# Optimization experiments

Measured on AMD Instinct MI355X. Metric: run time of the kernel, lower is better.

Reference implementation:

```python
import jax, jax.numpy as jnp
import numpy as np

B, C, D, T = 64, 1024, 32, 32
F4 = C // 4
GLOBAL_MARGIN = 0.2
MAX_VIOLATION = True
EPS = 1e-8


def setup_inputs() -> dict:
    key = jax.random.key(0)
    k = jax.random.split(key, 8)
    videos = jax.random.normal(k[0], (B, C, D, T), jnp.float32)
    sentences = jax.random.normal(k[1], (B, C), jnp.float32)
    lam = jnp.full((1,), 0.3, jnp.float32)
    mask = jnp.ones((B, D, T), jnp.int32)
    iou_maps = jax.random.uniform(k[2], (D * T, D * T), dtype=jnp.float32)
    lim = float(np.sqrt(6.0 / (C + F4)))  # xavier_uniform for Linear(C, C//4)
    W_v = jax.random.uniform(k[3], (4, C, F4), jnp.float32, -lim, lim)
    b_v = jnp.zeros((4, F4), jnp.float32)
    W_s = jax.random.uniform(k[4], (4, C, F4), jnp.float32, -lim, lim)
    b_s = jnp.zeros((4, F4), jnp.float32)
    return dict(videos=videos, sentences=sentences, lam=lam, mask=mask,
                iou_maps=iou_maps, valid_num=50,
                W_v=W_v, b_v=b_v, W_s=W_s, b_s=b_s)


def _forward(videos, sentences, W_v, b_v, W_s, b_s, lam, mask, iou_maps, valid_num):
    b, c, d, t = videos.shape
    # per-sample channel-mean centering
    videos = videos - jnp.mean(videos, axis=1, keepdims=True)
    sentences = sentences - jnp.mean(sentences, axis=1, keepdims=True)
    # 4-way linear projections, concatenated back along channel dim
    v = jnp.transpose(videos, (0, 2, 3, 1))                      # [b,d,t,c]
    v_cat = (jnp.einsum('bdtc,kcf->bkfdt', v, W_v)
             + b_v[None, :, :, None, None]).reshape(b, c, d, t)  # [b,c,d,t]
    s_cat = (jnp.einsum('bc,kcf->bkf', sentences, W_s) + b_s[None]).reshape(b, c)
    # cosine similarity over channel dim, vectorized over the batch loop
    vn = v_cat / jnp.maximum(jnp.linalg.norm(v_cat, axis=1, keepdims=True), EPS)
    sn = s_cat / jnp.maximum(jnp.linalg.norm(s_cat, axis=1, keepdims=True), EPS)
    sim = jnp.einsum('bcdt,sc->sbdt', vn, sn)                    # [s,b,d,t]
    sim = jnp.where(mask[None] == 0, -jnp.inf, sim)
    positive_map = sim[jnp.arange(b), jnp.arange(b)]             # [b,d,t]
    # top-k proposals + soft-NMS suppression (get_video_score_nms)
    flat = sim.reshape(b, b, d * t)
    vals, idx = jax.lax.top_k(flat, valid_num)                   # [s,b,v]
    iou_sub = iou_maps[idx[..., :, None], idx[..., None, :]]     # [s,b,v,v]
    tril = jnp.tril(jnp.ones((valid_num, valid_num), vals.dtype), -1)
    penalty = jnp.einsum('sblk,lk->sbk', iou_sub * iou_sub, tril)
    w = jnp.exp(-penalty / lam[0])                               # gaussian soft-NMS weight
    scores = jnp.mean(vals * w, axis=-1)                         # [s,b]
    # margin-based contrastive loss on the b x b score matrix
    diag = jnp.diagonal(scores)
    cost_s = jnp.clip(GLOBAL_MARGIN + scores - diag[:, None], 0.0)
    cost_im = jnp.clip(GLOBAL_MARGIN + scores - diag[None, :], 0.0)
    eye = jnp.eye(b, dtype=bool)
    cost_s = jnp.where(eye, 0.0, cost_s)
    cost_im = jnp.where(eye, 0.0, cost_im)
    if MAX_VIOLATION:
        cost_s = cost_s.max(axis=1)
        cost_im = cost_im.max(axis=0)
    loss = cost_s.sum() / b + cost_im.sum() / b
    return loss, positive_map


def reference(videos, sentences, lam, mask, iou_maps, valid_num, W_v, b_v, W_s, b_s):
    return _forward(videos, sentences, W_v, b_v, W_s, b_s, lam, mask, iou_maps, valid_num)
```

## Files before the change

kernel.cpp:

```cpp
#include <hip/hip_runtime.h>
#include <cstdint>
#include <cstddef>

#define CDIM  1024
#define DTDIM 1024
#define MDIM  65536
#define BDIM  64
#define VNUM  50

typedef __attribute__((ext_vector_type(8))) short bf16x8;
typedef __attribute__((ext_vector_type(4))) float f32x4;

__device__ __forceinline__ float bf2f(unsigned int u16) {
  return __uint_as_float(u16 << 16);
}
__device__ __forceinline__ unsigned short f2bf(float x) {
  unsigned int u = __float_as_uint(x);
  u += 0x7fffu + ((u >> 16) & 1u);
  return (unsigned short)(u >> 16);
}

__device__ __forceinline__ void gload16(const void* g, void* l) {
  __builtin_amdgcn_global_load_lds((const __attribute__((address_space(1))) void*)g,
                                   (__attribute__((address_space(3))) void*)l,
                                   16, 0, 0);
}

__global__ void k_transpose_videos(const float* __restrict__ vid,
                                   unsigned short* __restrict__ At,
                                   float* __restrict__ vsums) {
  __shared__ float t[64][65];
  const int tid = threadIdx.x;
  const int dt0 = blockIdx.x * 64, c0 = blockIdx.y * 64, b = blockIdx.z;
  const int lc = tid >> 4;
  const int l4 = (tid & 15) * 4;
  const float* src = vid + ((size_t)b * CDIM + c0) * DTDIM + dt0;
#pragma unroll
  for (int p = 0; p < 4; p++) {
    const int c = p * 16 + lc;
    const float4 f = *reinterpret_cast<const float4*>(&src[(size_t)c * DTDIM + l4]);
    t[c][l4 + 0] = f.x; t[c][l4 + 1] = f.y; t[c][l4 + 2] = f.z; t[c][l4 + 3] = f.w;
  }
  __syncthreads();
  const int dr = tid >> 5;
  const int cl = tid & 31;
  unsigned int* dstbase = reinterpret_cast<unsigned int*>(
      At + ((size_t)(b * DTDIM + dt0)) * CDIM + c0);
#pragma unroll
  for (int p = 0; p < 8; p++) {
    const int dt = p * 8 + dr;
    const float a0 = t[2 * cl][dt], a1 = t[2 * cl + 1][dt];
    const unsigned int u = (unsigned int)f2bf(a0) | ((unsigned int)f2bf(a1) << 16);
    dstbase[(size_t)dt * 512 + cl] = u;
    float s = a0 + a1;
    s += __shfl_xor(s, 1);  s += __shfl_xor(s, 2);  s += __shfl_xor(s, 4);
    s += __shfl_xor(s, 8);  s += __shfl_xor(s, 16);
    if (cl == 0) atomicAdd(&vsums[(size_t)b * DTDIM + dt0 + dt], s);
  }
}

__global__ void k_transpose_W(const float* __restrict__ W,
                              unsigned short* __restrict__ Wt) {
  __shared__ float t[32][33];
  const int tx = threadIdx.x & 31, ty = threadIdx.x >> 5;
  const int f0 = blockIdx.x * 32, c0 = blockIdx.y * 32, kb = blockIdx.z;
  const float* src = W + ((size_t)kb * CDIM + c0) * 256 + f0;
#pragma unroll
  for (int i = 0; i < 4; i++) {
    const int cl = ty + i * 8;
    t[cl][tx] = src[(size_t)cl * 256 + tx];
  }
  __syncthreads();
  unsigned short* dst = Wt + ((size_t)(kb * 256 + f0)) * CDIM + c0;
#pragma unroll
  for (int i = 0; i < 4; i++) {
    const int fl = ty + i * 8;
    dst[(size_t)fl * CDIM + tx] = f2bf(t[tx][fl]);
  }
}

__global__ void k_row_sums(const unsigned short* __restrict__ A,
                           float* __restrict__ out, int nrows) {
  const int wave = threadIdx.x >> 6, lane = threadIdx.x & 63;
  const int row = blockIdx.x * 4 + wave;
  if (row >= nrows) return;
  const unsigned short* r = A + (size_t)row * 1024;
  float s = 0.f;
#pragma unroll
  for (int h = 0; h < 2; h++) {
    const uint4 u = *reinterpret_cast<const uint4*>(r + h * 512 + lane * 8);
    s += bf2f(u.x & 0xffffu) + bf2f(u.x >> 16);
    s += bf2f(u.y & 0xffffu) + bf2f(u.y >> 16);
    s += bf2f(u.z & 0xffffu) + bf2f(u.z >> 16);
    s += bf2f(u.w & 0xffffu) + bf2f(u.w >> 16);
  }
#pragma unroll
  for (int o = 32; o; o >>= 1) s += __shfl_down(s, o);
  if (lane == 0) out[row] = s;
}

__global__ void k_scat(const float* __restrict__ sent, const float* __restrict__ Ws,
                       const float* __restrict__ bs, unsigned short* __restrict__ scat,
                       float* __restrict__ snorm2) {
  const int s = blockIdx.x, j = blockIdx.y, tid = threadIdx.x;
  __shared__ float sc[1024];
  __shared__ float red[4];
  float p = 0.f;
#pragma unroll
  for (int q = 0; q < 4; q++) {
    const float x = sent[(size_t)s * 1024 + tid + q * 256];
    sc[tid + q * 256] = x;
    p += x;
  }
#pragma unroll
  for (int o = 32; o; o >>= 1) p += __shfl_down(p, o);
  const int wave = tid >> 6, lane = tid & 63;
  if (lane == 0) red[wave] = p;
  __syncthreads();
  const float mean = (red[0] + red[1] + red[2] + red[3]) * (1.f / 1024.f);
  float acc = 0.f;
  const float* W = Ws + ((size_t)j * 1024) * 256 + tid;
  for (int c = 0; c < 1024; c++) acc += (sc[c] - mean) * W[(size_t)c * 256];
  const int n = j * 256 + tid;
  const float val = acc + bs[n];
  scat[(size_t)s * 1024 + n] = f2bf(val);
  float v2 = val * val;
#pragma unroll
  for (int o = 32; o; o >>= 1) v2 += __shfl_down(v2, o);
  if (lane == 0) atomicAdd(&snorm2[s], v2);
}

__global__ void k_gemm1(const unsigned short* __restrict__ At,
                        const unsigned short* __restrict__ Wt,
                        const float* __restrict__ vsums, const float* __restrict__ csW,
                        const float* __restrict__ bv,
                        unsigned short* __restrict__ vcat, float* __restrict__ vnorm2) {
  __shared__ alignas(16) unsigned short sA[128 * 32];
  __shared__ alignas(16) unsigned short sB[128 * 32];
  const int tid = threadIdx.x;
  const int wave = tid >> 6, lane = tid & 63;
  const int quad = lane >> 4, l16 = lane & 15;
  const int id = blockIdx.x;
  const int m0 = (((id >> 6) << 3) + (id & 7)) * 128;
  const int n0 = ((id >> 3) & 7) * 128;
  const int wm = (wave & 1) * 64, wn = (wave >> 1) * 64;

  f32x4 acc[4][4];
#pragma unroll
  for (int i = 0; i < 4; i++)
#pragma unroll
    for (int j = 0; j < 4; j++) acc[i][j] = f32x4{0.f, 0.f, 0.f, 0.f};

  const int r = lane >> 2;
  const int kk = (((lane & 3) ^ ((r >> 1) & 3)) * 8);
  const int rowA0 = (wave * 2 + 0) * 16 + r;
  const int rowA1 = (wave * 2 + 1) * 16 + r;
  const unsigned short* gA0 = At + (size_t)(m0 + rowA0) * CDIM + kk;
  const unsigned short* gA1 = At + (size_t)(m0 + rowA1) * CDIM + kk;
  const unsigned short* gB0 = Wt + (size_t)(n0 + rowA0) * CDIM + kk;
  const unsigned short* gB1 = Wt + (size_t)(n0 + rowA1) * CDIM + kk;
  unsigned short* lA0 = &sA[(wave * 2 + 0) * 512];
  unsigned short* lA1 = &sA[(wave * 2 + 1) * 512];
  unsigned short* lB0 = &sB[(wave * 2 + 0) * 512];
  unsigned short* lB1 = &sB[(wave * 2 + 1) * 512];

  const int sw = (l16 >> 1) & 3;

  for (int kt = 0; kt < 32; ++kt) {
    const int koff = kt * 32;
    gload16(gA0 + koff, lA0);
    gload16(gA1 + koff, lA1);
    gload16(gB0 + koff, lB0);
    gload16(gB1 + koff, lB1);
    __syncthreads();
    bf16x8 aF[4], bF[4];
#pragma unroll
    for (int i = 0; i < 4; i++)
      aF[i] = *reinterpret_cast<const bf16x8*>(
          &sA[(wm + i * 16 + l16) * 32 + ((quad ^ sw) * 8)]);
#pragma unroll
    for (int j = 0; j < 4; j++)
      bF[j] = *reinterpret_cast<const bf16x8*>(
          &sB[(wn + j * 16 + l16) * 32 + ((quad ^ sw) * 8)]);
#pragma unroll
    for (int i = 0; i < 4; i++)
#pragma unroll
      for (int j = 0; j < 4; j++)
        acc[i][j] = __builtin_amdgcn_mfma_f32_16x16x32_bf16(aF[i], bF[j], acc[i][j], 0, 0, 0);
    __syncthreads();
  }

  const float inv1024 = 1.f / 1024.f;
#pragma unroll
  for (int i = 0; i < 4; i++) {
    const int rbase = m0 + wm + i * 16 + quad * 4;
    const float4 vs = *reinterpret_cast<const float4*>(&vsums[rbase]);
    const float mu[4] = {vs.x * inv1024, vs.y * inv1024, vs.z * inv1024, vs.w * inv1024};
    float ss[4] = {0.f, 0.f, 0.f, 0.f};
#pragma unroll
    for (int j = 0; j < 4; j++) {
      const int col = n0 + wn + j * 16 + l16;
      const float cs = csW[col];
      const float bb = bv[col];
#pragma unroll
      for (int rr = 0; rr < 4; rr++) {
        const float val = acc[i][j][rr] - mu[rr] * cs + bb;
        vcat[(size_t)(rbase + rr) * CDIM + col] = f2bf(val);
        ss[rr] += val * val;
      }
    }
#pragma unroll
    for (int rr = 0; rr < 4; rr++) {
      float v = ss[rr];
      v += __shfl_xor(v, 1); v += __shfl_xor(v, 2);
      v += __shfl_xor(v, 4); v += __shfl_xor(v, 8);
      if (l16 == 0) atomicAdd(&vnorm2[rbase + rr], v);
    }
  }
}

__global__ void k_gemm2(const unsigned short* __restrict__ scat,
                        const unsigned short* __restrict__ vcat,
                        const float* __restrict__ snorm2, const float* __restrict__ vnorm2,
                        const int* __restrict__ mask,
                        float* __restrict__ sim, float* __restrict__ pm) {
  __shared__ alignas(16) unsigned short sS[64 * 32];
  __shared__ alignas(16) unsigned short sV[128 * 32];
  const int tid = threadIdx.x;
  const int wave = tid >> 6, lane = tid & 63;
  const int quad = lane >> 4, l16 = lane & 15;
  const int m0 = blockIdx.x * 128;

  f32x4 acc[4][2];
#pragma unroll
  for (int i = 0; i < 4; i++)
#pragma unroll
    for (int j = 0; j < 2; j++) acc[i][j] = f32x4{0.f, 0.f, 0.f, 0.f};

  const int r = lane >> 2;
  const int kk = (((lane & 3) ^ ((r >> 1) & 3)) * 8);
  const int rS = wave * 16 + r;
  const int rV0 = (wave * 2 + 0) * 16 + r;
  const int rV1 = (wave * 2 + 1) * 16 + r;
  const unsigned short* gS = scat + (size_t)rS * CDIM + kk;
  const unsigned short* gV0 = vcat + (size_t)(m0 + rV0) * CDIM + kk;
  const unsigned short* gV1 = vcat + (size_t)(m0 + rV1) * CDIM + kk;
  unsigned short* lS = &sS[wave * 512];
  unsigned short* lV0 = &sV[(wave * 2 + 0) * 512];
  unsigned short* lV1 = &sV[(wave * 2 + 1) * 512];

  const int sw = (l16 >> 1) & 3;

  for (int kt = 0; kt < 32; ++kt) {
    const int koff = kt * 32;
    gload16(gS + koff, lS);
    gload16(gV0 + koff, lV0);
    gload16(gV1 + koff, lV1);
    __syncthreads();
    bf16x8 aF[4], bF[2];
#pragma unroll
    for (int i = 0; i < 4; i++)
      aF[i] = *reinterpret_cast<const bf16x8*>(
          &sS[(i * 16 + l16) * 32 + ((quad ^ sw) * 8)]);
#pragma unroll
    for (int j = 0; j < 2; j++)
      bF[j] = *reinterpret_cast<const bf16x8*>(
          &sV[(wave * 32 + j * 16 + l16) * 32 + ((quad ^ sw) * 8)]);
#pragma unroll
    for (int i = 0; i < 4; i++)
#pragma unroll
      for (int j = 0; j < 2; j++)
        acc[i][j] = __builtin_amdgcn_mfma_f32_16x16x32_bf16(aF[i], bF[j], acc[i][j], 0, 0, 0);
    __syncthreads();
  }

  const int b0 = m0 >> 10;
#pragma unroll
  for (int j = 0; j < 2; j++) {
    const int m = m0 + wave * 32 + j * 16 + l16;
    const float vn = fmaxf(sqrtf(vnorm2[m]), 1e-8f);
    const int mk = mask[m];
#pragma unroll
    for (int i = 0; i < 4; i++) {
#pragma unroll
      for (int rr = 0; rr < 4; rr++) {
        const int s = i * 16 + quad * 4 + rr;
        const float sn = fmaxf(sqrtf(snorm2[s]), 1e-8f);
        float val = acc[i][j][rr] / (vn * sn);
        if (mk == 0) val = -__builtin_inff();
        sim[(size_t)s * MDIM + m] = val;
        if (s == b0) pm[m] = val;
      }
    }
  }
}

__global__ void k_topk(const float* __restrict__ sim, const float* __restrict__ iou,
                       const float* __restrict__ lam, float* __restrict__ scores) {
  const int wave = threadIdx.x >> 6, lane = threadIdx.x & 63;
  const int sb = blockIdx.x * 4 + wave;
  const int s = sb >> 6, b = sb & 63;
  __shared__ float tvs[4][VNUM];
  __shared__ int tis[4][VNUM];

  const float* row = sim + (size_t)s * MDIM + (size_t)b * 1024;
  float v[16];
#pragma unroll
  for (int j = 0; j < 16; j++) v[j] = row[j * 64 + lane];

  for (int k = 0; k < VNUM; k++) {
    float bv = v[0]; int bj = 0;
#pragma unroll
    for (int j = 1; j < 16; j++)
      if (v[j] > bv) { bv = v[j]; bj = j; }
    int bidx = bj * 64 + lane;
#pragma unroll
    for (int o = 1; o < 64; o <<= 1) {
      const float ov = __shfl_xor(bv, o);
      const int oi = __shfl_xor(bidx, o);
      if (ov > bv || (ov == bv && oi < bidx)) { bv = ov; bidx = oi; }
    }
    if (lane == 0) { tvs[wave][k] = bv; tis[wave][k] = bidx; }
    const int wj = bidx >> 6;
    const bool mine = (bidx & 63) == lane;
#pragma unroll
    for (int j = 0; j < 16; j++)
      if (mine && wj == j) v[j] = -__builtin_inff();
  }
  __syncthreads();

  float contrib = 0.f;
  if (lane < VNUM) {
    const int myidx = tis[wave][lane];
    float pen = 0.f;
    for (int l = lane + 1; l < VNUM; l++) {
      const float u = iou[(size_t)tis[wave][l] * 1024 + myidx];
      pen += u * u;
    }
    contrib = tvs[wave][lane] * expf(-pen / lam[0]);
  }
#pragma unroll
  for (int o = 32; o; o >>= 1) contrib += __shfl_down(contrib, o);
  if (lane == 0) scores[s * 64 + b] = contrib * (1.f / VNUM);
}

__global__ void k_loss(const float* __restrict__ scores, float* __restrict__ out) {
  __shared__ float S[64 * 64];
  __shared__ float diag[64];
  __shared__ float rmax[64], cmax[64];
  const int tid = threadIdx.x;
#pragma unroll
  for (int q = 0; q < 16; q++) S[tid + q * 256] = scores[tid + q * 256];
  __syncthreads();
  if (tid < 64) diag[tid] = S[tid * 64 + tid];
  __syncthreads();
  if (tid < 64) {
    float rm = 0.f, cm = 0.f;
    for (int x = 0; x < 64; x++) {
      if (x != tid) {
        const float cs = 0.2f + S[tid * 64 + x] - diag[tid];
        rm = fmaxf(rm, fmaxf(cs, 0.f));
        const float ci = 0.2f + S[x * 64 + tid] - diag[tid];
        cm = fmaxf(cm, fmaxf(ci, 0.f));
      }
    }
    rmax[tid] = rm; cmax[tid] = cm;
  }
  __syncthreads();
  if (tid == 0) {
    float L = 0.f;
    for (int t = 0; t < 64; t++) L += rmax[t] + cmax[t];
    out[0] = L * (1.f / 64.f);
  }
}

extern "C" void kernel_launch(void* const* d_in, const int* in_sizes, int n_in,
                              void* d_out, int out_size, void* d_ws, size_t ws_size,
                              hipStream_t stream) {
  (void)in_sizes; (void)n_in; (void)out_size; (void)ws_size;
  const float* videos = (const float*)d_in[0];
  const float* sent   = (const float*)d_in[1];
  const float* lam    = (const float*)d_in[2];
  const int*   mask   = (const int*)d_in[3];
  const float* iou    = (const float*)d_in[4];
  const float* W_v    = (const float*)d_in[6];
  const float* b_v    = (const float*)d_in[7];
  const float* W_s    = (const float*)d_in[8];
  const float* b_s    = (const float*)d_in[9];
  float* out = (float*)d_out;

  char* ws = (char*)d_ws;
  unsigned short* At   = (unsigned short*)(ws + 0);
  unsigned short* vcat = (unsigned short*)(ws + 134217728);
  float* sim           = (float*)(ws + 268435456);
  unsigned short* Wt   = (unsigned short*)(ws + 285212672);
  unsigned short* scat = (unsigned short*)(ws + 287309824);
  float* vsums         = (float*)(ws + 287440896);
  float* vnorm2        = (float*)(ws + 287703040);
  float* snorm2        = (float*)(ws + 287965184);
  float* csW           = (float*)(ws + 287965440);
  float* scores        = (float*)(ws + 287969536);

  hipMemsetAsync(vsums, 0, 262144 + 262144 + 256, stream);

  k_transpose_videos<<<dim3(16, 16, 64), 256, 0, stream>>>(videos, At, vsums);
  k_transpose_W<<<dim3(8, 32, 4), 256, 0, stream>>>(W_v, Wt);
  k_row_sums<<<256, 256, 0, stream>>>(Wt, csW, 1024);
  k_scat<<<dim3(64, 4), 256, 0, stream>>>(sent, W_s, b_s, scat, snorm2);
  k_gemm1<<<dim3(4096), 256, 0, stream>>>(At, Wt, vsums, csW, b_v, vcat, vnorm2);
  k_gemm2<<<dim3(512), 256, 0, stream>>>(scat, vcat, snorm2, vnorm2, mask, sim, out + 1);
  k_topk<<<dim3(1024), 256, 0, stream>>>(sim, iou, lam, scores);
  k_loss<<<1, 256, 0, stream>>>(scores, out);
}
```

Measured before the change: 742.9 us.

## Fuse projection GEMM and similarity GEMM, keeping vcat tiles in LDS

The two GEMMs are merged into one kernel. Each block computes a 128-row slab of the projected video features one 128-column tile at a time, stores the bf16 tile in LDS and immediately multiplies it against the matching slice of the sentence embeddings. This removes the 128 MB vcat intermediate (its global write and re-read), the vnorm2 atomics and one launch. The K step grows to 64, and norms are combined through LDS and reciprocals. In exchange the grid shrinks to 512 blocks with no double buffering and heavier LDS use, which may cut latency hiding for the large first GEMM.

Measured after the change: 725.9 us. 1.02x faster.

```diff
diff --git a/kernel.cpp b/kernel.cpp
--- a/kernel.cpp
+++ b/kernel.cpp
@@ -130,166 +130,156 @@
   if (lane == 0) atomicAdd(&snorm2[s], v2);
 }
 
-__global__ void k_gemm1(const unsigned short* __restrict__ At,
-                        const unsigned short* __restrict__ Wt,
-                        const float* __restrict__ vsums, const float* __restrict__ csW,
-                        const float* __restrict__ bv,
-                        unsigned short* __restrict__ vcat, float* __restrict__ vnorm2) {
-  __shared__ alignas(16) unsigned short sA[128 * 32];
-  __shared__ alignas(16) unsigned short sB[128 * 32];
-  const int tid = threadIdx.x;
-  const int wave = tid >> 6, lane = tid & 63;
-  const int quad = lane >> 4, l16 = lane & 15;
-  const int id = blockIdx.x;
-  const int m0 = (((id >> 6) << 3) + (id & 7)) * 128;
-  const int n0 = ((id >> 3) & 7) * 128;
-  const int wm = (wave & 1) * 64, wn = (wave >> 1) * 64;
-
-  f32x4 acc[4][4];
-#pragma unroll
-  for (int i = 0; i < 4; i++)
-#pragma unroll
-    for (int j = 0; j < 4; j++) acc[i][j] = f32x4{0.f, 0.f, 0.f, 0.f};
-
-  const int r = lane >> 2;
-  const int kk = (((lane & 3) ^ ((r >> 1) & 3)) * 8);
-  const int rowA0 = (wave * 2 + 0) * 16 + r;
-  const int rowA1 = (wave * 2 + 1) * 16 + r;
-  const unsigned short* gA0 = At + (size_t)(m0 + rowA0) * CDIM + kk;
-  const unsigned short* gA1 = At + (size_t)(m0 + rowA1) * CDIM + kk;
-  const unsigned short* gB0 = Wt + (size_t)(n0 + rowA0) * CDIM + kk;
-  const unsigned short* gB1 = Wt + (size_t)(n0 + rowA1) * CDIM + kk;
-  unsigned short* lA0 = &sA[(wave * 2 + 0) * 512];
-  unsigned short* lA1 = &sA[(wave * 2 + 1) * 512];
-  unsigned short* lB0 = &sB[(wave * 2 + 0) * 512];
-  unsigned short* lB1 = &sB[(wave * 2 + 1) * 512];
-
-  const int sw = (l16 >> 1) & 3;
-
-  for (int kt = 0; kt < 32; ++kt) {
-    const int koff = kt * 32;
-    gload16(gA0 + koff, lA0);
-    gload16(gA1 + koff, lA1);
-    gload16(gB0 + koff, lB0);
-    gload16(gB1 + koff, lB1);
-    __syncthreads();
-    bf16x8 aF[4], bF[4];
-#pragma unroll
-    for (int i = 0; i < 4; i++)
-      aF[i] = *reinterpret_cast<const bf16x8*>(
-          &sA[(wm + i * 16 + l16) * 32 + ((quad ^ sw) * 8)]);
-#pragma unroll
-    for (int j = 0; j < 4; j++)
-      bF[j] = *reinterpret_cast<const bf16x8*>(
-          &sB[(wn + j * 16 + l16) * 32 + ((quad ^ sw) * 8)]);
-#pragma unroll
-    for (int i = 0; i < 4; i++)
-#pragma unroll
-      for (int j = 0; j < 4; j++)
-        acc[i][j] = __builtin_amdgcn_mfma_f32_16x16x32_bf16(aF[i], bF[j], acc[i][j], 0, 0, 0);
-    __syncthreads();
-  }
-
-  const float inv1024 = 1.f / 1024.f;
-#pragma unroll
-  for (int i = 0; i < 4; i++) {
-    const int rbase = m0 + wm + i * 16 + quad * 4;
-    const float4 vs = *reinterpret_cast<const float4*>(&vsums[rbase]);
-    const float mu[4] = {vs.x * inv1024, vs.y * inv1024, vs.z * inv1024, vs.w * inv1024};
-    float ss[4] = {0.f, 0.f, 0.f, 0.f};
-#pragma unroll
-    for (int j = 0; j < 4; j++) {
-      const int col = n0 + wn + j * 16 + l16;
-      const float cs = csW[col];
-      const float bb = bv[col];
-#pragma unroll
-      for (int rr = 0; rr < 4; rr++) {
-        const float val = acc[i][j][rr] - mu[rr] * cs + bb;
-        vcat[(size_t)(rbase + rr) * CDIM + col] = f2bf(val);
-        ss[rr] += val * val;
-      }
-    }
-#pragma unroll
-    for (int rr = 0; rr < 4; rr++) {
-      float v = ss[rr];
-      v += __shfl_xor(v, 1); v += __shfl_xor(v, 2);
-      v += __shfl_xor(v, 4); v += __shfl_xor(v, 8);
-      if (l16 == 0) atomicAdd(&vnorm2[rbase + rr], v);
-    }
-  }
-}
-
-__global__ void k_gemm2(const unsigned short* __restrict__ scat,
-                        const unsigned short* __restrict__ vcat,
-                        const float* __restrict__ snorm2, const float* __restrict__ vnorm2,
-                        const int* __restrict__ mask,
-                        float* __restrict__ sim, float* __restrict__ pm) {
-  __shared__ alignas(16) unsigned short sS[64 * 32];
-  __shared__ alignas(16) unsigned short sV[128 * 32];
+__global__ __launch_bounds__(256, 2) void k_gemm_fused(
+    const unsigned short* __restrict__ At, const unsigned short* __restrict__ Wt,
+    const float* __restrict__ vsums, const float* __restrict__ csW,
+    const float* __restrict__ bv, const unsigned short* __restrict__ scat,
+    const float* __restrict__ snorm2, const int* __restrict__ mask,
+    float* __restrict__ sim, float* __restrict__ pm) {
+  __shared__ alignas(16) char smem[32768 + 16384 + 256 + 1024];
+  unsigned short* sAB   = (unsigned short*)smem;
+  unsigned short* vtile = (unsigned short*)smem;
+  unsigned short* stile = (unsigned short*)(smem + 32768);
+  float* invSnLds       = (float*)(smem + 49152);
+  float* vnLds          = (float*)(smem + 49152 + 256);
+
   const int tid = threadIdx.x;
   const int wave = tid >> 6, lane = tid & 63;
   const int quad = lane >> 4, l16 = lane & 15;
   const int m0 = blockIdx.x * 128;
-
-  f32x4 acc[4][2];
+  const int wm = (wave & 1) * 64, wn = (wave >> 1) * 64;
+
+  if (tid < 64) invSnLds[tid] = 1.f / fmaxf(sqrtf(snorm2[tid]), 1e-8f);
+
+  f32x4 acc2[4][2];
 #pragma unroll
   for (int i = 0; i < 4; i++)
 #pragma unroll
-    for (int j = 0; j < 2; j++) acc[i][j] = f32x4{0.f, 0.f, 0.f, 0.f};
-
-  const int r = lane >> 2;
-  const int kk = (((lane & 3) ^ ((r >> 1) & 3)) * 8);
-  const int rS = wave * 16 + r;
-  const int rV0 = (wave * 2 + 0) * 16 + r;
-  const int rV1 = (wave * 2 + 1) * 16 + r;
-  const unsigned short* gS = scat + (size_t)rS * CDIM + kk;
-  const unsigned short* gV0 = vcat + (size_t)(m0 + rV0) * CDIM + kk;
-  const unsigned short* gV1 = vcat + (size_t)(m0 + rV1) * CDIM + kk;
-  unsigned short* lS = &sS[wave * 512];
-  unsigned short* lV0 = &sV[(wave * 2 + 0) * 512];
-  unsigned short* lV1 = &sV[(wave * 2 + 1) * 512];
-
-  const int sw = (l16 >> 1) & 3;
-
-  for (int kt = 0; kt < 32; ++kt) {
-    const int koff = kt * 32;
-    gload16(gS + koff, lS);
-    gload16(gV0 + koff, lV0);
-    gload16(gV1 + koff, lV1);
+    for (int j = 0; j < 2; j++) acc2[i][j] = f32x4{0.f, 0.f, 0.f, 0.f};
+  float ss[4][4];
+#pragma unroll
+  for (int i = 0; i < 4; i++)
+#pragma unroll
+    for (int rr = 0; rr < 4; rr++) ss[i][rr] = 0.f;
+
+  const float inv1024 = 1.f / 1024.f;
+
+  for (int nt = 0; nt < 8; ++nt) {
+    const int n0 = nt * 128;
+
+#pragma unroll
+    for (int ii = 0; ii < 4; ii++) {
+      const int srow = (ii * 4 + wave) * 4 + (lane >> 4);
+      const int g = (lane & 15) ^ (srow & 15);
+      gload16(scat + (size_t)srow * 1024 + n0 + g * 8,
+              stile + (ii * 4 + wave) * 512);
+    }
+
+    f32x4 acc[4][4];
+#pragma unroll
+    for (int i = 0; i < 4; i++)
+#pragma unroll
+      for (int j = 0; j < 4; j++) acc[i][j] = f32x4{0.f, 0.f, 0.f, 0.f};
+
+    for (int kt = 0; kt < 16; ++kt) {
+      const int koff = kt * 64;
+#pragma unroll
+      for (int ii = 0; ii < 4; ii++) {
+        const int r = (ii * 4 + wave) * 8 + (lane >> 3);
+        const int g = (lane & 7) ^ (r & 7);
+        gload16(At + (size_t)(m0 + r) * CDIM + koff + g * 8,
+                sAB + (ii * 4 + wave) * 512);
+        gload16(Wt + (size_t)(n0 + r) * CDIM + koff + g * 8,
+                sAB + 8192 + (ii * 4 + wave) * 512);
+      }
+      __syncthreads();
+#pragma unroll
+      for (int ks = 0; ks < 2; ks++) {
+        const int slot = ((ks * 4 + quad) ^ (l16 & 7)) * 8;
+        bf16x8 aF[4], bF[4];
+#pragma unroll
+        for (int i = 0; i < 4; i++)
+          aF[i] = *reinterpret_cast<const bf16x8*>(&sAB[(wm + i * 16 + l16) * 64 + slot]);
+#pragma unroll
+        for (int j = 0; j < 4; j++)
+          bF[j] = *reinterpret_cast<const bf16x8*>(&sAB[8192 + (wn + j * 16 + l16) * 64 + slot]);
+#pragma unroll
+        for (int i = 0; i < 4; i++)
+#pragma unroll
+          for (int j = 0; j < 4; j++)
+            acc[i][j] = __builtin_amdgcn_mfma_f32_16x16x32_bf16(aF[i], bF[j], acc[i][j], 0, 0, 0);
+      }
+      __syncthreads();
+    }
+
+#pragma unroll
+    for (int i = 0; i < 4; i++) {
+      const int rbase = wm + i * 16 + quad * 4;
+      const float4 vs = *reinterpret_cast<const float4*>(&vsums[m0 + rbase]);
+      const float mu[4] = {vs.x * inv1024, vs.y * inv1024, vs.z * inv1024, vs.w * inv1024};
+#pragma unroll
+      for (int j = 0; j < 4; j++) {
+        const int c = wn + j * 16 + l16;
+        const float cs = csW[n0 + c];
+        const float bb = bv[n0 + c];
+#pragma unroll
+        for (int rr = 0; rr < 4; rr++) {
+          const int m = rbase + rr;
+          const float val = acc[i][j][rr] - mu[rr] * cs + bb;
+          ss[i][rr] += val * val;
+          const int slot = (c >> 3) ^ (m & 15);
+          vtile[m * 128 + slot * 8 + (c & 7)] = f2bf(val);
+        }
+      }
+    }
     __syncthreads();
-    bf16x8 aF[4], bF[2];
-#pragma unroll
-    for (int i = 0; i < 4; i++)
-      aF[i] = *reinterpret_cast<const bf16x8*>(
-          &sS[(i * 16 + l16) * 32 + ((quad ^ sw) * 8)]);
-#pragma unroll
-    for (int j = 0; j < 2; j++)
-      bF[j] = *reinterpret_cast<const bf16x8*>(
-          &sV[(wave * 32 + j * 16 + l16) * 32 + ((quad ^ sw) * 8)]);
-#pragma unroll
-    for (int i = 0; i < 4; i++)
-#pragma unroll
-      for (int j = 0; j < 2; j++)
-        acc[i][j] = __builtin_amdgcn_mfma_f32_16x16x32_bf16(aF[i], bF[j], acc[i][j], 0, 0, 0);
+
+#pragma unroll
+    for (int ks2 = 0; ks2 < 4; ks2++) {
+      const int slot = ((ks2 * 4 + quad) ^ l16) * 8;
+      bf16x8 a2[4], b2[2];
+#pragma unroll
+      for (int i2 = 0; i2 < 4; i2++)
+        a2[i2] = *reinterpret_cast<const bf16x8*>(&stile[(i2 * 16 + l16) * 128 + slot]);
+#pragma unroll
+      for (int j2 = 0; j2 < 2; j2++)
+        b2[j2] = *reinterpret_cast<const bf16x8*>(&vtile[(wave * 32 + j2 * 16 + l16) * 128 + slot]);
+#pragma unroll
+      for (int i2 = 0; i2 < 4; i2++)
+#pragma unroll
+        for (int j2 = 0; j2 < 2; j2++)
+          acc2[i2][j2] = __builtin_amdgcn_mfma_f32_16x16x32_bf16(a2[i2], b2[j2], acc2[i2][j2], 0, 0, 0);
+    }
     __syncthreads();
   }
 
+#pragma unroll
+  for (int i = 0; i < 4; i++)
+#pragma unroll
+    for (int rr = 0; rr < 4; rr++) {
+      float v = ss[i][rr];
+      v += __shfl_xor(v, 1); v += __shfl_xor(v, 2);
+      v += __shfl_xor(v, 4); v += __shfl_xor(v, 8);
+      if (l16 == 0) vnLds[(wave >> 1) * 128 + wm + i * 16 + quad * 4 + rr] = v;
+    }
+  __syncthreads();
+
   const int b0 = m0 >> 10;
 #pragma unroll
-  for (int j = 0; j < 2; j++) {
-    const int m = m0 + wave * 32 + j * 16 + l16;
-    const float vn = fmaxf(sqrtf(vnorm2[m]), 1e-8f);
-    const int mk = mask[m];
-#pragma unroll
-    for (int i = 0; i < 4; i++) {
-#pragma unroll
-      for (int rr = 0; rr < 4; rr++) {
-        const int s = i * 16 + quad * 4 + rr;
-        const float sn = fmaxf(sqrtf(snorm2[s]), 1e-8f);
-        float val = acc[i][j][rr] / (vn * sn);
+  for (int j2 = 0; j2 < 2; j2++) {
+    const int ml = wave * 32 + j2 * 16 + l16;
+    const float nv = vnLds[ml] + vnLds[128 + ml];
+    const float invVn = 1.f / fmaxf(sqrtf(nv), 1e-8f);
+    const int mk = mask[m0 + ml];
+#pragma unroll
+    for (int i2 = 0; i2 < 4; i2++) {
+#pragma unroll
+      for (int reg = 0; reg < 4; reg++) {
+        const int s = i2 * 16 + quad * 4 + reg;
+        float val = acc2[i2][j2][reg] * invVn * invSnLds[s];
         if (mk == 0) val = -__builtin_inff();
-        sim[(size_t)s * MDIM + m] = val;
-        if (s == b0) pm[m] = val;
+        sim[(size_t)s * MDIM + m0 + ml] = val;
+        if (s == b0) pm[m0 + ml] = val;
       }
     }
   }
@@ -391,24 +381,22 @@
 
   char* ws = (char*)d_ws;
   unsigned short* At   = (unsigned short*)(ws + 0);
-  unsigned short* vcat = (unsigned short*)(ws + 134217728);
-  float* sim           = (float*)(ws + 268435456);
-  unsigned short* Wt   = (unsigned short*)(ws + 285212672);
-  unsigned short* scat = (unsigned short*)(ws + 287309824);
-  float* vsums         = (float*)(ws + 287440896);
-  float* vnorm2        = (float*)(ws + 287703040);
-  float* snorm2        = (float*)(ws + 287965184);
-  float* csW           = (float*)(ws + 287965440);
-  float* scores        = (float*)(ws + 287969536);
-
-  hipMemsetAsync(vsums, 0, 262144 + 262144 + 256, stream);
+  float* sim           = (float*)(ws + 134217728);
+  unsigned short* Wt   = (unsigned short*)(ws + 150994944);
+  unsigned short* scat = (unsigned short*)(ws + 153092096);
+  float* vsums         = (float*)(ws + 153223168);
+  float* snorm2        = (float*)(ws + 153485312);
+  float* csW           = (float*)(ws + 153485568);
+  float* scores        = (float*)(ws + 153489664);
+
+  hipMemsetAsync(vsums, 0, 262144 + 256, stream);
 
   k_transpose_videos<<<dim3(16, 16, 64), 256, 0, stream>>>(videos, At, vsums);
   k_transpose_W<<<dim3(8, 32, 4), 256, 0, stream>>>(W_v, Wt);
   k_row_sums<<<256, 256, 0, stream>>>(Wt, csW, 1024);
   k_scat<<<dim3(64, 4), 256, 0, stream>>>(sent, W_s, b_s, scat, snorm2);
-  k_gemm1<<<dim3(4096), 256, 0, stream>>>(At, Wt, vsums, csW, b_v, vcat, vnorm2);
-  k_gemm2<<<dim3(512), 256, 0, stream>>>(scat, vcat, snorm2, vnorm2, mask, sim, out + 1);
+  k_gemm_fused<<<dim3(512), 256, 0, stream>>>(At, Wt, vsums, csW, b_v, scat,
+                                              snorm2, mask, sim, out + 1);
   k_topk<<<dim3(1024), 256, 0, stream>>>(sim, iou, lam, scores);
   k_loss<<<1, 256, 0, stream>>>(scores, out);
 }
```
